# Performance work log

Measured on AMD Instinct MI355X. Metric: run time of the kernel, lower is better.

Reference implementation:

```python
import jax, jax.numpy as jnp
import numpy as np

B, H, S, D = 2, 16, 2048, 64
SOFTCLAMP = 50.0


def setup_inputs() -> dict:
    key = jax.random.key(0)
    kq, kk, kv, km = jax.random.split(key, 4)
    q = jax.random.normal(kq, (B, H, S, D), dtype=jnp.float32)
    k = jax.random.normal(kk, (B, H, S, D), dtype=jnp.float32)
    v = jax.random.normal(kv, (B, H, S, D), dtype=jnp.float32)
    mask = jax.random.randint(km, (B, S), 0, 2).astype(jnp.bool_)
    return {"q": q, "k": k, "v": v, "mask": mask}


def reference(q, k, v, mask):
    scale = q.shape[-1] ** -0.5
    # [b, h, i, j] similarity logits
    sim = jnp.einsum('bhid,bhjd->bhij', q, k) * scale
    # tanh-based logit softclamping (Gemma2-style softcapping)
    sim = jnp.tanh(sim / SOFTCLAMP) * SOFTCLAMP
    mask_value = -jnp.finfo(sim.dtype).max
    sim = jnp.where(mask[:, None, None, :], sim, mask_value)
    attn = jax.nn.softmax(sim, axis=-1)
    out = jnp.einsum('bhij,bhjd->bhid', attn, v)
    return out, attn
```

## Files before the change

### kernel.cpp

```cpp
#include <hip/hip_runtime.h>
#include <hip/hip_bf16.h>

#define B_ 2
#define H_ 16
#define S_ 2048
#define D_ 64
#define BUFSTR 72
#define BUFSZ (16 * BUFSTR)

typedef float f32x4 __attribute__((ext_vector_type(4)));
typedef short s16x8 __attribute__((ext_vector_type(8)));
typedef short s16x4 __attribute__((ext_vector_type(4)));

__device__ __forceinline__ short f2bf(float f) {
  unsigned u = __float_as_uint(f);
  u += 0x7FFFu + ((u >> 16) & 1u);
  return (short)(u >> 16);
}
__device__ __forceinline__ float bf2f(short s) {
  return __uint_as_float(((unsigned)(unsigned short)s) << 16);
}

__device__ __forceinline__ float softcap_p(float a) {
  const float k1 = 0.18033688011f;
  const float k2 = -3.7570183e-07f;
  const float k3 = 9.3926761e-13f;
  const float C  = 72.134752044f;
  float y = a * a;
  float t = __builtin_fmaf(y, k3, k2);
  t = __builtin_fmaf(y, t, k1);
  float arg = __builtin_fmaf(a, t, -C);
  arg = fminf(arg, 0.f);
  return exp2f(arg);
}

__global__ __launch_bounds__(256) void prep_k(const float* __restrict__ k,
                                              short* __restrict__ kbf) {
  size_t i = ((size_t)blockIdx.x * 256 + threadIdx.x) * 8;
  const f32x4* ka = (const f32x4*)(k + i);
  f32x4 b0 = __builtin_nontemporal_load(ka);
  f32x4 b1 = __builtin_nontemporal_load(ka + 1);
  s16x8 ok;
  #pragma unroll
  for (int e = 0; e < 4; ++e) { ok[e] = f2bf(b0[e]); ok[4 + e] = f2bf(b1[e]); }
  *(s16x8*)(kbf + i) = ok;
}

__global__ __launch_bounds__(256) void prep_v(const float* __restrict__ v,
                                              short* __restrict__ vt) {
  __shared__ float tile[64][65];
  const int tid = threadIdx.x;
  const int j0 = blockIdx.x * 64;
  const int bh = blockIdx.y;
  const float* vh = v + (size_t)bh * S_ * D_;
  #pragma unroll
  for (int it = 0; it < 16; ++it) {
    int idx = it * 256 + tid;
    int row = idx >> 6, col = idx & 63;
    tile[row][col] = __builtin_nontemporal_load(&vh[(size_t)(j0 + row) * D_ + col]);
  }
  __syncthreads();
  short* vth = vt + (size_t)bh * D_ * S_;
  #pragma unroll
  for (int it = 0; it < 16; ++it) {
    int idx = it * 256 + tid;
    int d = idx >> 6, jj = idx & 63;
    vth[(size_t)d * S_ + j0 + jj] = f2bf(tile[jj][d]);
  }
}

template <bool PRE>
__global__ __launch_bounds__(256, 4) void attend_wave(
    const float* __restrict__ q, const float* __restrict__ k,
    const float* __restrict__ v, const int* __restrict__ mask,
    const short* __restrict__ kbf, const short* __restrict__ vt,
    float* __restrict__ out, float* __restrict__ attn) {
  __shared__ short ldsbuf[4 * BUFSZ];
  const int tid = threadIdx.x, wv = tid >> 6, lane = tid & 63;
  const int lg = lane >> 4, li = lane & 15;

  const unsigned flat = blockIdx.x;
  const unsigned xcd = flat & 7, idx = flat >> 3;
  const int bh = (int)(xcd * 4 + (idx >> 5));
  const int q0 = (int)(idx & 31) * 64 + wv * 16;
  const int b  = bh >> 4;
  const int* mrow = mask + (size_t)b * S_;
  short* myb = ldsbuf + wv * BUFSZ;

  s16x8 qf0, qf1;
  {
    const float* qr = q + ((size_t)bh * S_ + q0 + li) * D_ + lg * 8;
    #pragma unroll
    for (int e = 0; e < 8; ++e) { qf0[e] = f2bf(qr[e]); qf1[e] = f2bf(qr[32 + e]); }
  }

  const short* kb = PRE ? (kbf + (size_t)bh * S_ * D_) : nullptr;
  const short* vb = PRE ? (vt + (size_t)bh * D_ * S_) : nullptr;

  float rs[4] = {0.f, 0.f, 0.f, 0.f};
  #pragma unroll 2
  for (int c = 0; c < 32; ++c) {
    const int jc = c * 64;
    f32x4 acc[4];
    #pragma unroll
    for (int n = 0; n < 4; ++n) acc[n] = (f32x4){0.f, 0.f, 0.f, 0.f};
    #pragma unroll
    for (int n = 0; n < 4; ++n) {
      if constexpr (PRE) {
        const short* kr = kb + (size_t)(jc + n * 16 + li) * D_ + lg * 8;
        acc[n] = __builtin_amdgcn_mfma_f32_16x16x32_bf16(qf0, *(const s16x8*)kr, acc[n], 0, 0, 0);
        acc[n] = __builtin_amdgcn_mfma_f32_16x16x32_bf16(qf1, *(const s16x8*)(kr + 32), acc[n], 0, 0, 0);
      } else {
        const float* kr = k + ((size_t)bh * S_ + jc + n * 16 + li) * D_ + lg * 8;
        s16x8 k0, k1;
        #pragma unroll
        for (int e = 0; e < 8; ++e) { k0[e] = f2bf(kr[e]); k1[e] = f2bf(kr[32 + e]); }
        acc[n] = __builtin_amdgcn_mfma_f32_16x16x32_bf16(qf0, k0, acc[n], 0, 0, 0);
        acc[n] = __builtin_amdgcn_mfma_f32_16x16x32_bf16(qf1, k1, acc[n], 0, 0, 0);
      }
    }
    #pragma unroll
    for (int n = 0; n < 4; ++n) {
      const bool keep = mrow[jc + n * 16 + li] != 0;
      #pragma unroll
      for (int r = 0; r < 4; ++r) {
        float p = softcap_p(acc[n][r]);
        rs[r] += keep ? p : 0.f;
      }
    }
  }
  #pragma unroll
  for (int r = 0; r < 4; ++r) {
    rs[r] += __shfl_xor(rs[r], 1, 64);
    rs[r] += __shfl_xor(rs[r], 2, 64);
    rs[r] += __shfl_xor(rs[r], 4, 64);
    rs[r] += __shfl_xor(rs[r], 8, 64);
  }
  float rinv4[4];
  #pragma unroll
  for (int r = 0; r < 4; ++r) rinv4[r] = (rs[r] > 0.f) ? 1.f / rs[r] : 0.f;

  f32x4 pvacc[4];
  #pragma unroll
  for (int m = 0; m < 4; ++m) pvacc[m] = (f32x4){0.f, 0.f, 0.f, 0.f};
  float* abase = attn + ((size_t)bh * S_ + q0) * S_;

  #pragma unroll 2
  for (int c = 0; c < 32; ++c) {
    const int jc = c * 64;
    f32x4 acc[4];
    #pragma unroll
    for (int n = 0; n < 4; ++n) acc[n] = (f32x4){0.f, 0.f, 0.f, 0.f};
    #pragma unroll
    for (int n = 0; n < 4; ++n) {
      if constexpr (PRE) {
        const short* kr = kb + (size_t)(jc + n * 16 + li) * D_ + lg * 8;
        acc[n] = __builtin_amdgcn_mfma_f32_16x16x32_bf16(qf0, *(const s16x8*)kr, acc[n], 0, 0, 0);
        acc[n] = __builtin_amdgcn_mfma_f32_16x16x32_bf16(qf1, *(const s16x8*)(kr + 32), acc[n], 0, 0, 0);
      } else {
        const float* kr = k + ((size_t)bh * S_ + jc + n * 16 + li) * D_ + lg * 8;
        s16x8 k0, k1;
        #pragma unroll
        for (int e = 0; e < 8; ++e) { k0[e] = f2bf(kr[e]); k1[e] = f2bf(kr[32 + e]); }
        acc[n] = __builtin_amdgcn_mfma_f32_16x16x32_bf16(qf0, k0, acc[n], 0, 0, 0);
        acc[n] = __builtin_amdgcn_mfma_f32_16x16x32_bf16(qf1, k1, acc[n], 0, 0, 0);
      }
    }

    #pragma unroll
    for (int n = 0; n < 4; ++n) {
      const bool keep = mrow[jc + n * 16 + li] != 0;
      const int col = n * 16 + li;
      #pragma unroll
      for (int r = 0; r < 4; ++r) {
        float p = softcap_p(acc[n][r]);
        float pn = (keep ? p : 0.f) * rinv4[r];
        myb[(lg * 4 + r) * BUFSTR + col] = f2bf(pn);
      }
    }

    #pragma unroll
    for (int ks = 0; ks < 2; ++ks) {
      s16x8 pa = *(const s16x8*)&myb[li * BUFSTR + ks * 32 + lg * 8];
      #pragma unroll
      for (int m = 0; m < 4; ++m) {
        s16x8 vf;
        if constexpr (PRE) {
          vf = *(const s16x8*)(vb + (size_t)(m * 16 + li) * S_ + jc + ks * 32 + lg * 8);
        } else {
          const float* vp = v + (size_t)bh * S_ * D_ + (size_t)(jc + ks * 32 + lg * 8) * D_ + m * 16 + li;
          #pragma unroll
          for (int e = 0; e < 8; ++e) vf[e] = f2bf(vp[(size_t)e * D_]);
        }
        pvacc[m] = __builtin_amdgcn_mfma_f32_16x16x32_bf16(pa, vf, pvacc[m], 0, 0, 0);
      }
    }

    #pragma unroll
    for (int rr = 0; rr < 4; ++rr) {
      const int row = rr * 4 + lg;
      s16x4 pb = *(const s16x4*)&myb[row * BUFSTR + li * 4];
      f32x4 a;
      a[0] = bf2f(pb[0]); a[1] = bf2f(pb[1]);
      a[2] = bf2f(pb[2]); a[3] = bf2f(pb[3]);
      __builtin_nontemporal_store(a, (f32x4*)(abase + (size_t)row * S_ + jc + li * 4));
    }
  }

  #pragma unroll
  for (int m = 0; m < 4; ++m)
    #pragma unroll
    for (int r = 0; r < 4; ++r)
      out[((size_t)bh * S_ + q0 + lg * 4 + r) * D_ + m * 16 + li] = pvacc[m][r];
}

extern "C" void kernel_launch(void* const* d_in, const int* in_sizes, int n_in,
                              void* d_out, int out_size, void* d_ws, size_t ws_size,
                              hipStream_t stream) {
  const float* q = (const float*)d_in[0];
  const float* k = (const float*)d_in[1];
  const float* v = (const float*)d_in[2];
  const int* mask = (const int*)d_in[3];

  float* out  = (float*)d_out;
  const size_t nel = (size_t)B_ * H_ * S_ * D_;
  float* attn = out + nel;

  const size_t need = nel * 2 * 2;

  if (ws_size >= need) {
    short* kbf = (short*)d_ws;
    short* vtp = kbf + nel;
    prep_k<<<(int)(nel / (256 * 8)), 256, 0, stream>>>(k, kbf);
    prep_v<<<dim3(S_ / 64, B_ * H_), 256, 0, stream>>>(v, vtp);
    attend_wave<true><<<1024, 256, 0, stream>>>(q, k, v, mask, kbf, vtp, out, attn);
  } else {
    attend_wave<false><<<1024, 256, 0, stream>>>(q, k, v, mask, nullptr, nullptr, out, attn);
  }
}
```

Measured before the change: 384.5 us.

## Split key dimension across eight waves per query tile with LDS reductions

Restructures the attention kernel so each 512-thread block handles 16 queries, with 8 waves splitting the 2048 keys. Row sums and PV partial outputs are reduced across waves through shared memory. The K and V prep kernels are fused into one launch, the exp uses the raw hardware exp2 without clamping, and attn stores become regular instead of nontemporal. This raises parallelism and occupancy, and the per-wave loop drops from 32 chunks to 4, at the cost of extra syncs and LDS reductions.

```diff
diff --git a/kernel.cpp b/kernel.cpp
--- a/kernel.cpp
+++ b/kernel.cpp
@@ -30,62 +30,67 @@
   float t = __builtin_fmaf(y, k3, k2);
   t = __builtin_fmaf(y, t, k1);
   float arg = __builtin_fmaf(a, t, -C);
-  arg = fminf(arg, 0.f);
-  return exp2f(arg);
-}
-
-__global__ __launch_bounds__(256) void prep_k(const float* __restrict__ k,
-                                              short* __restrict__ kbf) {
-  size_t i = ((size_t)blockIdx.x * 256 + threadIdx.x) * 8;
-  const f32x4* ka = (const f32x4*)(k + i);
-  f32x4 b0 = __builtin_nontemporal_load(ka);
-  f32x4 b1 = __builtin_nontemporal_load(ka + 1);
-  s16x8 ok;
-  #pragma unroll
-  for (int e = 0; e < 4; ++e) { ok[e] = f2bf(b0[e]); ok[4 + e] = f2bf(b1[e]); }
-  *(s16x8*)(kbf + i) = ok;
-}
-
-__global__ __launch_bounds__(256) void prep_v(const float* __restrict__ v,
-                                              short* __restrict__ vt) {
-  __shared__ float tile[64][65];
-  const int tid = threadIdx.x;
-  const int j0 = blockIdx.x * 64;
-  const int bh = blockIdx.y;
-  const float* vh = v + (size_t)bh * S_ * D_;
-  #pragma unroll
-  for (int it = 0; it < 16; ++it) {
-    int idx = it * 256 + tid;
-    int row = idx >> 6, col = idx & 63;
-    tile[row][col] = __builtin_nontemporal_load(&vh[(size_t)(j0 + row) * D_ + col]);
-  }
-  __syncthreads();
-  short* vth = vt + (size_t)bh * D_ * S_;
-  #pragma unroll
-  for (int it = 0; it < 16; ++it) {
-    int idx = it * 256 + tid;
-    int d = idx >> 6, jj = idx & 63;
-    vth[(size_t)d * S_ + j0 + jj] = f2bf(tile[jj][d]);
+  return __builtin_amdgcn_exp2f(arg);
+}
+
+#define KBLK ((B_ * H_ * S_ * D_) / (256 * 8))
+__global__ __launch_bounds__(256) void prep_kv(const float* __restrict__ k,
+                                               const float* __restrict__ v,
+                                               short* __restrict__ kbf,
+                                               short* __restrict__ vt) {
+  if ((int)blockIdx.x < KBLK) {
+    size_t i = ((size_t)blockIdx.x * 256 + threadIdx.x) * 8;
+    const f32x4* ka = (const f32x4*)(k + i);
+    f32x4 b0 = __builtin_nontemporal_load(ka);
+    f32x4 b1 = __builtin_nontemporal_load(ka + 1);
+    s16x8 ok;
+    #pragma unroll
+    for (int e = 0; e < 4; ++e) { ok[e] = f2bf(b0[e]); ok[4 + e] = f2bf(b1[e]); }
+    *(s16x8*)(kbf + i) = ok;
+  } else {
+    __shared__ float tile[64][65];
+    const int blk = (int)blockIdx.x - KBLK;
+    const int j0 = (blk & 31) * 64;
+    const int bh = blk >> 5;
+    const int tid = threadIdx.x;
+    const float* vh = v + (size_t)bh * S_ * D_;
+    #pragma unroll
+    for (int it = 0; it < 16; ++it) {
+      int idx = it * 256 + tid;
+      int row = idx >> 6, col = idx & 63;
+      tile[row][col] = __builtin_nontemporal_load(&vh[(size_t)(j0 + row) * D_ + col]);
+    }
+    __syncthreads();
+    short* vth = vt + (size_t)bh * D_ * S_;
+    #pragma unroll
+    for (int it = 0; it < 16; ++it) {
+      int idx = it * 256 + tid;
+      int d = idx >> 6, jj = idx & 63;
+      vth[(size_t)d * S_ + j0 + jj] = f2bf(tile[jj][d]);
+    }
   }
 }
 
 template <bool PRE>
-__global__ __launch_bounds__(256, 4) void attend_wave(
+__global__ __launch_bounds__(512, 8) void attend_hiocc(
     const float* __restrict__ q, const float* __restrict__ k,
     const float* __restrict__ v, const int* __restrict__ mask,
     const short* __restrict__ kbf, const short* __restrict__ vt,
     float* __restrict__ out, float* __restrict__ attn) {
-  __shared__ short ldsbuf[4 * BUFSZ];
+  __shared__ float pvred[8][16][64];
+  __shared__ float ls_rs[8][16];
+  __shared__ float ls_rinv[16];
+
   const int tid = threadIdx.x, wv = tid >> 6, lane = tid & 63;
   const int lg = lane >> 4, li = lane & 15;
 
-  const unsigned flat = blockIdx.x;
-  const unsigned xcd = flat & 7, idx = flat >> 3;
-  const int bh = (int)(xcd * 4 + (idx >> 5));
-  const int q0 = (int)(idx & 31) * 64 + wv * 16;
+  const unsigned flat = blockIdx.y * gridDim.x + blockIdx.x;
+  const unsigned swz  = (flat & 7) * 512 + (flat >> 3);
+  const int q0 = (int)(swz & 127) * 16;
+  const int bh = (int)(swz >> 7);
   const int b  = bh >> 4;
   const int* mrow = mask + (size_t)b * S_;
-  short* myb = ldsbuf + wv * BUFSZ;
+  short* myb = (short*)pvred + wv * BUFSZ;
 
   s16x8 qf0, qf1;
   {
@@ -98,9 +103,9 @@
   const short* vb = PRE ? (vt + (size_t)bh * D_ * S_) : nullptr;
 
   float rs[4] = {0.f, 0.f, 0.f, 0.f};
-  #pragma unroll 2
-  for (int c = 0; c < 32; ++c) {
-    const int jc = c * 64;
+  #pragma unroll 1
+  for (int c = 0; c < 4; ++c) {
+    const int jc = c * 512 + wv * 64;
     f32x4 acc[4];
     #pragma unroll
     for (int n = 0; n < 4; ++n) acc[n] = (f32x4){0.f, 0.f, 0.f, 0.f};
@@ -129,6 +134,7 @@
       }
     }
   }
+
   #pragma unroll
   for (int r = 0; r < 4; ++r) {
     rs[r] += __shfl_xor(rs[r], 1, 64);
@@ -136,18 +142,31 @@
     rs[r] += __shfl_xor(rs[r], 4, 64);
     rs[r] += __shfl_xor(rs[r], 8, 64);
   }
+  if (li == 0) {
+    #pragma unroll
+    for (int r = 0; r < 4; ++r) ls_rs[wv][lg * 4 + r] = rs[r];
+  }
+  __syncthreads();
+  if (tid < 16) {
+    float ssum = 0.f;
+    #pragma unroll
+    for (int w = 0; w < 8; ++w) ssum += ls_rs[w][tid];
+    ls_rinv[tid] = (ssum > 0.f) ? 1.f / ssum : 0.f;
+  }
+  __syncthreads();
+
   float rinv4[4];
   #pragma unroll
-  for (int r = 0; r < 4; ++r) rinv4[r] = (rs[r] > 0.f) ? 1.f / rs[r] : 0.f;
+  for (int r = 0; r < 4; ++r) rinv4[r] = ls_rinv[lg * 4 + r];
 
   f32x4 pvacc[4];
   #pragma unroll
   for (int m = 0; m < 4; ++m) pvacc[m] = (f32x4){0.f, 0.f, 0.f, 0.f};
   float* abase = attn + ((size_t)bh * S_ + q0) * S_;
 
-  #pragma unroll 2
-  for (int c = 0; c < 32; ++c) {
-    const int jc = c * 64;
+  #pragma unroll 1
+  for (int c = 0; c < 4; ++c) {
+    const int jc = c * 512 + wv * 64;
     f32x4 acc[4];
     #pragma unroll
     for (int n = 0; n < 4; ++n) acc[n] = (f32x4){0.f, 0.f, 0.f, 0.f};
@@ -197,21 +216,34 @@
     }
 
     #pragma unroll
-    for (int rr = 0; rr < 4; ++rr) {
-      const int row = rr * 4 + lg;
+    for (int it = 0; it < 4; ++it) {
+      const int row = it * 4 + lg;
       s16x4 pb = *(const s16x4*)&myb[row * BUFSTR + li * 4];
       f32x4 a;
       a[0] = bf2f(pb[0]); a[1] = bf2f(pb[1]);
       a[2] = bf2f(pb[2]); a[3] = bf2f(pb[3]);
-      __builtin_nontemporal_store(a, (f32x4*)(abase + (size_t)row * S_ + jc + li * 4));
-    }
-  }
+      *(f32x4*)(abase + (size_t)row * S_ + jc + li * 4) = a;
+    }
+  }
+
+  __syncthreads();
 
   #pragma unroll
   for (int m = 0; m < 4; ++m)
     #pragma unroll
     for (int r = 0; r < 4; ++r)
-      out[((size_t)bh * S_ + q0 + lg * 4 + r) * D_ + m * 16 + li] = pvacc[m][r];
+      pvred[wv][lg * 4 + r][m * 16 + li] = pvacc[m][r];
+  __syncthreads();
+
+  #pragma unroll
+  for (int h = 0; h < 2; ++h) {
+    const int idx = h * 512 + tid;
+    const int qq = idx >> 6, d = idx & 63;
+    float ssum = 0.f;
+    #pragma unroll
+    for (int w = 0; w < 8; ++w) ssum += pvred[w][qq][d];
+    out[((size_t)bh * S_ + q0 + qq) * D_ + d] = ssum;
+  }
 }
 
 extern "C" void kernel_launch(void* const* d_in, const int* in_sizes, int n_in,
@@ -226,15 +258,15 @@
   const size_t nel = (size_t)B_ * H_ * S_ * D_;
   float* attn = out + nel;
 
+  dim3 grid(S_ / 16, B_ * H_);
   const size_t need = nel * 2 * 2;
 
   if (ws_size >= need) {
     short* kbf = (short*)d_ws;
     short* vtp = kbf + nel;
-    prep_k<<<(int)(nel / (256 * 8)), 256, 0, stream>>>(k, kbf);
-    prep_v<<<dim3(S_ / 64, B_ * H_), 256, 0, stream>>>(v, vtp);
-    attend_wave<true><<<1024, 256, 0, stream>>>(q, k, v, mask, kbf, vtp, out, attn);
+    prep_kv<<<KBLK + 32 * B_ * H_, 256, 0, stream>>>(k, v, kbf, vtp);
+    attend_hiocc<true><<<grid, 512, 0, stream>>>(q, k, v, mask, kbf, vtp, out, attn);
   } else {
-    attend_wave<false><<<1024, 256, 0, stream>>>(q, k, v, mask, nullptr, nullptr, out, attn);
-  }
-}
+    attend_hiocc<false><<<grid, 512, 0, stream>>>(q, k, v, mask, nullptr, nullptr, out, attn);
+  }
+}
```

Measured after the change: 410.5 us. 6.8% more time.
